# Optimization experiments

Measured on AMD Instinct MI355X. Metric: run time of the kernel, lower is better.

The kernel has to match this reference:

```python
import jax, jax.numpy as jnp
import numpy as np

DIM, HEADS = 512, 8
HD = DIM // HEADS
B, T = 1, 512


def _rope_tables(T, hd):
    inv_freq = 1.0 / (10000.0 ** (jnp.arange(0, hd, 2, dtype=jnp.float32) / hd))
    freqs = jnp.arange(T, dtype=jnp.float32)[:, None] * inv_freq[None, :]
    emb = jnp.concatenate([freqs, freqs], axis=-1)  # [T, hd]
    return jnp.cos(emb), jnp.sin(emb)


def _rotate_half_heads(x):
    # Faithful to source: torch chunk(2, dim=1) on [B,H,hd,1,T] splits the HEADS axis.
    x1, x2 = jnp.split(x, 2, axis=1)
    return jnp.concatenate([-x2, x1], axis=1)


def setup_inputs():
    key = jax.random.key(0)
    ks = jax.random.split(key, 5)
    s = 1.0 / np.sqrt(DIM)
    return {
        "x": jax.random.normal(ks[0], (B, T, DIM), dtype=jnp.float32),
        "Wq": jax.random.normal(ks[1], (DIM, DIM), dtype=jnp.float32) * s,
        "Wk": jax.random.normal(ks[2], (DIM, DIM), dtype=jnp.float32) * s,
        "Wv": jax.random.normal(ks[3], (DIM, DIM), dtype=jnp.float32) * s,
        "Wo": jax.random.normal(ks[4], (DIM, DIM), dtype=jnp.float32) * s,
    }


def reference(x, Wq, Wk, Wv, Wo):
    b, t, d = x.shape
    h, hd = HEADS, d // HEADS
    scale = 1.0 / np.sqrt(hd)

    def proj(W):
        # 1x1 Conv2d == per-position linear; channel o = head*hd + c  -> [B,H,hd,T]
        return jnp.einsum('btd,od->bot', x, W).reshape(b, h, hd, t)

    q, k, v = proj(Wq), proj(Wk), proj(Wv)

    cos, sin = _rope_tables(t, hd)
    cosT = cos.T[None, None]  # [1,1,hd,T]
    sinT = sin.T[None, None]
    q = q * cosT + _rotate_half_heads(q) * sinT
    k = k * cosT + _rotate_half_heads(k) * sinT

    # Per-channel outer-product scores (inner dim of the matmul is the singleton axis)
    att = jnp.einsum('bhci,bhcj->bhcij', q, k) * scale  # [B,H,hd,T,T]
    causal_mask = jnp.triu(jnp.ones((t, t), dtype=bool), k=1)
    att = jnp.where(causal_mask, -jnp.inf, att)
    att = jax.nn.softmax(att, axis=-1)

    out = jnp.einsum('bhcij,bhcj->bhci', att, v).reshape(b, d, t)
    return jnp.einsum('od,bdt->bto', Wo, out)  # [B,T,D]
```

## Files before the change

kernel.cpp:

```cpp
#include <hip/hip_runtime.h>
#include <math.h>

typedef __attribute__((ext_vector_type(8))) short short8;
typedef __attribute__((ext_vector_type(4))) float floatx4;

__device__ __forceinline__ unsigned short f2bf(float f) {
    unsigned int u = __builtin_bit_cast(unsigned int, f);
    u += 0x7FFFu + ((u >> 16) & 1u);
    return (unsigned short)(u >> 16);
}


__global__ __launch_bounds__(256) void cvt_bf16(
    const float* __restrict__ x,  const float* __restrict__ Wq,
    const float* __restrict__ Wk, const float* __restrict__ Wv,
    const float* __restrict__ Wo, unsigned short* __restrict__ Wallb,
    unsigned short* __restrict__ xb, unsigned short* __restrict__ Wob)
{
    const float* src; unsigned short* dst;
    switch (blockIdx.y) {
        case 0: src = Wq; dst = Wallb;          break;
        case 1: src = Wk; dst = Wallb + 262144; break;
        case 2: src = Wv; dst = Wallb + 524288; break;
        case 3: src = x;  dst = xb;             break;
        default: src = Wo; dst = Wob;           break;
    }
    const int i4 = (blockIdx.x * 256 + threadIdx.x) * 4;
    const float4 v = *(const float4*)(src + i4);
    ushort4 o;
    o.x = f2bf(v.x); o.y = f2bf(v.y); o.z = f2bf(v.z); o.w = f2bf(v.w);
    *(ushort4*)(dst + i4) = o;
}

__global__ __launch_bounds__(256) void gemm_bt(
    const unsigned short* __restrict__ A,
    const unsigned short* __restrict__ B,
    float* __restrict__ C)
{
    __shared__ unsigned short As[64 * 512];
    __shared__ unsigned short Bs[64 * 512];

    const int tid  = threadIdx.x;
    const int lane = tid & 63;
    const int w    = tid >> 6;
    const int m0   = blockIdx.y * 64;
    const int n0   = blockIdx.x * 64;
    const int wm   = (w >> 1) * 32;
    const int wn   = (w & 1) * 32;

    floatx4 acc[2][2] = {{{0.f,0.f,0.f,0.f},{0.f,0.f,0.f,0.f}},
                         {{0.f,0.f,0.f,0.f},{0.f,0.f,0.f,0.f}}};

    const int quad = lane >> 4;
    const int l15  = lane & 15;

    #pragma unroll
    for (int r = 0; r < 16; ++r) {
        const int row = w * 16 + r;
        const int col = (lane ^ (row & 7)) * 8;
        __builtin_amdgcn_global_load_lds(
            (const __attribute__((address_space(1))) void*)(A + (m0 + row) * 512 + col),
            (__attribute__((address_space(3))) void*)&As[row * 512],
            16, 0, 0);
        __builtin_amdgcn_global_load_lds(
            (const __attribute__((address_space(1))) void*)(B + (n0 + row) * 512 + col),
            (__attribute__((address_space(3))) void*)&Bs[row * 512],
            16, 0, 0);
    }

    asm volatile("s_waitcnt vmcnt(0)" ::: "memory");
    __builtin_amdgcn_s_barrier();
    __builtin_amdgcn_sched_barrier(0);

    #pragma unroll
    for (int kt = 0; kt < 8; ++kt) {
        #pragma unroll
        for (int ks = 0; ks < 2; ++ks) {
            const int cIdx = kt * 8 + ks * 4 + quad;
            short8 a[2], b[2];
            #pragma unroll
            for (int mt = 0; mt < 2; ++mt) {
                const int row = wm + mt * 16 + l15;
                a[mt] = *(const short8*)&As[row * 512 + ((cIdx ^ (row & 7)) * 8)];
            }
            #pragma unroll
            for (int nt = 0; nt < 2; ++nt) {
                const int row = wn + nt * 16 + l15;
                b[nt] = *(const short8*)&Bs[row * 512 + ((cIdx ^ (row & 7)) * 8)];
            }
            #pragma unroll
            for (int mt = 0; mt < 2; ++mt)
                #pragma unroll
                for (int nt = 0; nt < 2; ++nt)
                    acc[mt][nt] = __builtin_amdgcn_mfma_f32_16x16x32_bf16(
                        a[mt], b[nt], acc[mt][nt], 0, 0, 0);
        }
    }

    #pragma unroll
    for (int mt = 0; mt < 2; ++mt)
        #pragma unroll
        for (int nt = 0; nt < 2; ++nt) {
            const int grow = m0 + wm + mt * 16 + quad * 4;
            const int gcol = n0 + wn + nt * 16 + l15;
            #pragma unroll
            for (int r = 0; r < 4; ++r)
                C[(grow + r) * 512 + gcol] = acc[mt][nt][r];
        }
}

__global__ __launch_bounds__(256) void attn_rope(
    const float* __restrict__ qkv, unsigned short* __restrict__ attTb)
{
    const int ch = blockIdx.x;
    const int t  = threadIdx.x;
    const int i1 = t;
    const int i2 = 511 - t;
    const int p  = ch ^ 256;
    const float sgn = (ch < 256) ? -1.f : 1.f;

    __shared__ float ks_[512];
    __shared__ float vs_[512];

    const float* __restrict__ qg = qkv;
    const float* __restrict__ kg = qkv + 262144;
    const float* __restrict__ vg = qkv + 524288;

    const float inv_freq = powf(10000.f, -(float)(ch & 31) * (1.f / 32.f));
    const float SC = 0.125f * 1.44269504088896f;

    float sn_a, cs_a, sn_b, cs_b, sn_c, cs_c;
    sincosf((float)t * inv_freq,         &sn_a, &cs_a);
    sincosf((float)(t + 256) * inv_freq, &sn_b, &cs_b);
    sincosf((float)i2 * inv_freq,        &sn_c, &cs_c);

    ks_[t]       = (kg[ch * 512 + t]       * cs_a + sgn * kg[p * 512 + t]       * sn_a) * SC;
    ks_[t + 256] = (kg[ch * 512 + t + 256] * cs_b + sgn * kg[p * 512 + t + 256] * sn_b) * SC;
    vs_[t]       = vg[ch * 512 + t];
    vs_[t + 256] = vg[ch * 512 + t + 256];
    const float q1 = qg[ch * 512 + i1] * cs_a + sgn * qg[p * 512 + i1] * sn_a;
    const float q2 = qg[ch * 512 + i2] * cs_c + sgn * qg[p * 512 + i2] * sn_c;
    __syncthreads();

    float l1 = 0.f, a1 = 0.f, l2 = 0.f, a2 = 0.f;
    const int w64 = t & ~63;

    #pragma unroll 2
    for (int j = 0; j < w64; j += 4) {
        const float4 kk = *(const float4*)&ks_[j];
        const float4 vv = *(const float4*)&vs_[j];
        float e;
        e = __builtin_amdgcn_exp2f(q1 * kk.x); l1 += e; a1 = fmaf(e, vv.x, a1);
        e = __builtin_amdgcn_exp2f(q2 * kk.x); l2 += e; a2 = fmaf(e, vv.x, a2);
        e = __builtin_amdgcn_exp2f(q1 * kk.y); l1 += e; a1 = fmaf(e, vv.y, a1);
        e = __builtin_amdgcn_exp2f(q2 * kk.y); l2 += e; a2 = fmaf(e, vv.y, a2);
        e = __builtin_amdgcn_exp2f(q1 * kk.z); l1 += e; a1 = fmaf(e, vv.z, a1);
        e = __builtin_amdgcn_exp2f(q2 * kk.z); l2 += e; a2 = fmaf(e, vv.z, a2);
        e = __builtin_amdgcn_exp2f(q1 * kk.w); l1 += e; a1 = fmaf(e, vv.w, a1);
        e = __builtin_amdgcn_exp2f(q2 * kk.w); l2 += e; a2 = fmaf(e, vv.w, a2);
    }
    #pragma unroll 4
    for (int u = 0; u < 64; u += 4) {
        const int j = w64 + u;
        const float4 kk = *(const float4*)&ks_[j];
        const float4 vv = *(const float4*)&vs_[j];
        float e;
        e = (j + 0 <= i1) ? __builtin_amdgcn_exp2f(q1 * kk.x) : 0.f; l1 += e; a1 = fmaf(e, vv.x, a1);
        e = __builtin_amdgcn_exp2f(q2 * kk.x);                       l2 += e; a2 = fmaf(e, vv.x, a2);
        e = (j + 1 <= i1) ? __builtin_amdgcn_exp2f(q1 * kk.y) : 0.f; l1 += e; a1 = fmaf(e, vv.y, a1);
        e = __builtin_amdgcn_exp2f(q2 * kk.y);                       l2 += e; a2 = fmaf(e, vv.y, a2);
        e = (j + 2 <= i1) ? __builtin_amdgcn_exp2f(q1 * kk.z) : 0.f; l1 += e; a1 = fmaf(e, vv.z, a1);
        e = __builtin_amdgcn_exp2f(q2 * kk.z);                       l2 += e; a2 = fmaf(e, vv.z, a2);
        e = (j + 3 <= i1) ? __builtin_amdgcn_exp2f(q1 * kk.w) : 0.f; l1 += e; a1 = fmaf(e, vv.w, a1);
        e = __builtin_amdgcn_exp2f(q2 * kk.w);                       l2 += e; a2 = fmaf(e, vv.w, a2);
    }
    const int jend2 = 448 - w64;
    #pragma unroll 2
    for (int j = w64 + 64; j < jend2; j += 4) {
        const float4 kk = *(const float4*)&ks_[j];
        const float4 vv = *(const float4*)&vs_[j];
        float e;
        e = __builtin_amdgcn_exp2f(q2 * kk.x); l2 += e; a2 = fmaf(e, vv.x, a2);
        e = __builtin_amdgcn_exp2f(q2 * kk.y); l2 += e; a2 = fmaf(e, vv.y, a2);
        e = __builtin_amdgcn_exp2f(q2 * kk.z); l2 += e; a2 = fmaf(e, vv.z, a2);
        e = __builtin_amdgcn_exp2f(q2 * kk.w); l2 += e; a2 = fmaf(e, vv.w, a2);
    }
    #pragma unroll 4
    for (int u = 0; u < 64; u += 4) {
        const int j = jend2 + u;
        const float4 kk = *(const float4*)&ks_[j];
        const float4 vv = *(const float4*)&vs_[j];
        float e;
        e = (j + 0 <= i2) ? __builtin_amdgcn_exp2f(q2 * kk.x) : 0.f; l2 += e; a2 = fmaf(e, vv.x, a2);
        e = (j + 1 <= i2) ? __builtin_amdgcn_exp2f(q2 * kk.y) : 0.f; l2 += e; a2 = fmaf(e, vv.y, a2);
        e = (j + 2 <= i2) ? __builtin_amdgcn_exp2f(q2 * kk.z) : 0.f; l2 += e; a2 = fmaf(e, vv.z, a2);
        e = (j + 3 <= i2) ? __builtin_amdgcn_exp2f(q2 * kk.w) : 0.f; l2 += e; a2 = fmaf(e, vv.w, a2);
    }

    attTb[i1 * 512 + ch] = f2bf(a1 / l1);
    attTb[i2 * 512 + ch] = f2bf(a2 / l2);
}

extern "C" void kernel_launch(void* const* d_in, const int* in_sizes, int n_in,
                              void* d_out, int out_size, void* d_ws, size_t ws_size,
                              hipStream_t stream)
{
    const float* x  = (const float*)d_in[0];
    const float* Wq = (const float*)d_in[1];
    const float* Wk = (const float*)d_in[2];
    const float* Wv = (const float*)d_in[3];
    const float* Wo = (const float*)d_in[4];
    float* out = (float*)d_out;

    unsigned short* Wallb = (unsigned short*)d_ws;
    unsigned short* xb    = Wallb + 786432;
    unsigned short* Wob   = xb + 262144;
    unsigned short* attTb = Wob + 262144;
    float* qkvf = (float*)(attTb + 262144);

    cvt_bf16<<<dim3(256, 5), 256, 0, stream>>>(x, Wq, Wk, Wv, Wo, Wallb, xb, Wob);
    gemm_bt<<<dim3(8, 24), 256, 0, stream>>>(Wallb, xb, qkvf);
    attn_rope<<<512, 256, 0, stream>>>(qkvf, attTb);
    gemm_bt<<<dim3(8, 8), 256, 0, stream>>>(attTb, Wob, out);
}
```

Before: 92.75 us.

## Fuse fp32-to-bf16 conversion into GEMM tile staging, drop separate convert kernel

Removes the standalone cvt_bf16 kernel and converts fp32 inputs to bf16 while staging GEMM tiles into shared memory, using packed v_cvt_pk_bf16_f32 instructions. The QKV GEMM now reads Wq/Wk/Wv and x directly as fp32, and the output GEMM converts Wo on the fly. This saves one launch and a round trip through bf16 workspace buffers. In exchange, each tile reads twice as many bytes, the async global_load_lds path is lost for converted operands, and tiles are re-converted redundantly across blocks.

```diff
diff --git a/kernel.cpp b/kernel.cpp
--- a/kernel.cpp
+++ b/kernel.cpp
@@ -11,30 +11,24 @@
 }
 
 
-__global__ __launch_bounds__(256) void cvt_bf16(
-    const float* __restrict__ x,  const float* __restrict__ Wq,
-    const float* __restrict__ Wk, const float* __restrict__ Wv,
-    const float* __restrict__ Wo, unsigned short* __restrict__ Wallb,
-    unsigned short* __restrict__ xb, unsigned short* __restrict__ Wob)
-{
-    const float* src; unsigned short* dst;
-    switch (blockIdx.y) {
-        case 0: src = Wq; dst = Wallb;          break;
-        case 1: src = Wk; dst = Wallb + 262144; break;
-        case 2: src = Wv; dst = Wallb + 524288; break;
-        case 3: src = x;  dst = xb;             break;
-        default: src = Wo; dst = Wob;           break;
-    }
-    const int i4 = (blockIdx.x * 256 + threadIdx.x) * 4;
-    const float4 v = *(const float4*)(src + i4);
-    ushort4 o;
-    o.x = f2bf(v.x); o.y = f2bf(v.y); o.z = f2bf(v.z); o.w = f2bf(v.w);
-    *(ushort4*)(dst + i4) = o;
-}
-
-__global__ __launch_bounds__(256) void gemm_bt(
-    const unsigned short* __restrict__ A,
-    const unsigned short* __restrict__ B,
+__device__ __forceinline__ void stage_row_f32(
+    const float* __restrict__ src, unsigned short* __restrict__ dst,
+    int lane, int row)
+{
+    const float4 f0 = *(const float4*)(src + lane * 8);
+    const float4 f1 = *(const float4*)(src + lane * 8 + 4);
+    unsigned int p0, p1, p2, p3;
+    asm("v_cvt_pk_bf16_f32 %0, %1, %2" : "=v"(p0) : "v"(f0.x), "v"(f0.y));
+    asm("v_cvt_pk_bf16_f32 %0, %1, %2" : "=v"(p1) : "v"(f0.z), "v"(f0.w));
+    asm("v_cvt_pk_bf16_f32 %0, %1, %2" : "=v"(p2) : "v"(f1.x), "v"(f1.y));
+    asm("v_cvt_pk_bf16_f32 %0, %1, %2" : "=v"(p3) : "v"(f1.z), "v"(f1.w));
+    uint4 pk; pk.x = p0; pk.y = p1; pk.z = p2; pk.w = p3;
+    *(uint4*)&dst[(lane ^ (row & 7)) * 8] = pk;
+}
+
+__global__ __launch_bounds__(256) void gemm_qkv(
+    const float* __restrict__ Wq, const float* __restrict__ Wk,
+    const float* __restrict__ Wv, const float* __restrict__ x,
     float* __restrict__ C)
 {
     __shared__ unsigned short As[64 * 512];
@@ -48,6 +42,79 @@
     const int wm   = (w >> 1) * 32;
     const int wn   = (w & 1) * 32;
 
+    const float* __restrict__ Aall =
+        (m0 < 512) ? Wq : ((m0 < 1024) ? Wk : Wv);
+    const float* __restrict__ Asrc = Aall + (m0 & 511) * 512;
+    const float* __restrict__ Bsrc = x + n0 * 512;
+
+    floatx4 acc[2][2] = {{{0.f,0.f,0.f,0.f},{0.f,0.f,0.f,0.f}},
+                         {{0.f,0.f,0.f,0.f},{0.f,0.f,0.f,0.f}}};
+
+    const int quad = lane >> 4;
+    const int l15  = lane & 15;
+
+    #pragma unroll
+    for (int r = 0; r < 16; ++r) {
+        const int row = w * 16 + r;
+        stage_row_f32(Asrc + row * 512, &As[row * 512], lane, row);
+        stage_row_f32(Bsrc + row * 512, &Bs[row * 512], lane, row);
+    }
+    __syncthreads();
+    __builtin_amdgcn_sched_barrier(0);
+
+    #pragma unroll
+    for (int kt = 0; kt < 8; ++kt) {
+        #pragma unroll
+        for (int ks = 0; ks < 2; ++ks) {
+            const int cIdx = kt * 8 + ks * 4 + quad;
+            short8 a[2], b[2];
+            #pragma unroll
+            for (int mt = 0; mt < 2; ++mt) {
+                const int row = wm + mt * 16 + l15;
+                a[mt] = *(const short8*)&As[row * 512 + ((cIdx ^ (row & 7)) * 8)];
+            }
+            #pragma unroll
+            for (int nt = 0; nt < 2; ++nt) {
+                const int row = wn + nt * 16 + l15;
+                b[nt] = *(const short8*)&Bs[row * 512 + ((cIdx ^ (row & 7)) * 8)];
+            }
+            #pragma unroll
+            for (int mt = 0; mt < 2; ++mt)
+                #pragma unroll
+                for (int nt = 0; nt < 2; ++nt)
+                    acc[mt][nt] = __builtin_amdgcn_mfma_f32_16x16x32_bf16(
+                        a[mt], b[nt], acc[mt][nt], 0, 0, 0);
+        }
+    }
+
+    #pragma unroll
+    for (int mt = 0; mt < 2; ++mt)
+        #pragma unroll
+        for (int nt = 0; nt < 2; ++nt) {
+            const int grow = m0 + wm + mt * 16 + quad * 4;
+            const int gcol = n0 + wn + nt * 16 + l15;
+            #pragma unroll
+            for (int r = 0; r < 4; ++r)
+                C[(grow + r) * 512 + gcol] = acc[mt][nt][r];
+        }
+}
+
+__global__ __launch_bounds__(256) void gemm_out(
+    const unsigned short* __restrict__ A,
+    const float* __restrict__ B,
+    float* __restrict__ C)
+{
+    __shared__ unsigned short As[64 * 512];
+    __shared__ unsigned short Bs[64 * 512];
+
+    const int tid  = threadIdx.x;
+    const int lane = tid & 63;
+    const int w    = tid >> 6;
+    const int m0   = blockIdx.y * 64;
+    const int n0   = blockIdx.x * 64;
+    const int wm   = (w >> 1) * 32;
+    const int wn   = (w & 1) * 32;
+
     floatx4 acc[2][2] = {{{0.f,0.f,0.f,0.f},{0.f,0.f,0.f,0.f}},
                          {{0.f,0.f,0.f,0.f},{0.f,0.f,0.f,0.f}}};
 
@@ -62,14 +129,13 @@
             (const __attribute__((address_space(1))) void*)(A + (m0 + row) * 512 + col),
             (__attribute__((address_space(3))) void*)&As[row * 512],
             16, 0, 0);
-        __builtin_amdgcn_global_load_lds(
-            (const __attribute__((address_space(1))) void*)(B + (n0 + row) * 512 + col),
-            (__attribute__((address_space(3))) void*)&Bs[row * 512],
-            16, 0, 0);
-    }
-
-    asm volatile("s_waitcnt vmcnt(0)" ::: "memory");
-    __builtin_amdgcn_s_barrier();
+    }
+    #pragma unroll
+    for (int r = 0; r < 16; ++r) {
+        const int row = w * 16 + r;
+        stage_row_f32(B + (n0 + row) * 512, &Bs[row * 512], lane, row);
+    }
+    __syncthreads();
     __builtin_amdgcn_sched_barrier(0);
 
     #pragma unroll
@@ -212,14 +278,10 @@
     const float* Wo = (const float*)d_in[4];
     float* out = (float*)d_out;
 
-    unsigned short* Wallb = (unsigned short*)d_ws;
-    unsigned short* xb    = Wallb + 786432;
-    unsigned short* Wob   = xb + 262144;
-    unsigned short* attTb = Wob + 262144;
+    unsigned short* attTb = (unsigned short*)d_ws;
     float* qkvf = (float*)(attTb + 262144);
 
-    cvt_bf16<<<dim3(256, 5), 256, 0, stream>>>(x, Wq, Wk, Wv, Wo, Wallb, xb, Wob);
-    gemm_bt<<<dim3(8, 24), 256, 0, stream>>>(Wallb, xb, qkvf);
+    gemm_qkv<<<dim3(8, 24), 256, 0, stream>>>(Wq, Wk, Wv, x, qkvf);
     attn_rope<<<512, 256, 0, stream>>>(qkvf, attTb);
-    gemm_bt<<<dim3(8, 8), 256, 0, stream>>>(attTb, Wob, out);
-}
+    gemm_out<<<dim3(8, 8), 256, 0, stream>>>(attTb, Wo, out);
+}
```

Result: no change. 92.54 us (-0.2%).
